# Optimization experiments

Measured on AMD Instinct MI355X. Metric: run time of the kernel, lower is better.

## Reference

```python
import jax, jax.numpy as jnp
import numpy as np

NUM_HEADS = 32
NUM_KV_HEADS = 8
HEAD_DIM = 128
HIDDEN = 4096
B, L = 2, 4096


def _phi(x):
    # feature map: elu(x) + 1
    return jax.nn.elu(x) + 1.0


def setup_inputs() -> dict:
    key = jax.random.key(0)
    ks = jax.random.split(key, 9)
    s = 1.0 / np.sqrt(HIDDEN)
    return {
        "hidden_states": jax.random.normal(ks[0], (B, L, HIDDEN), jnp.float32),
        "Wq": jax.random.normal(ks[1], (HIDDEN, HIDDEN), jnp.float32) * s,
        "bq": jnp.zeros((HIDDEN,), jnp.float32),
        "Wk": jax.random.normal(ks[2], (NUM_KV_HEADS * HEAD_DIM, HIDDEN), jnp.float32) * s,
        "bk": jnp.zeros((NUM_KV_HEADS * HEAD_DIM,), jnp.float32),
        "Wv": jax.random.normal(ks[3], (NUM_KV_HEADS * HEAD_DIM, HIDDEN), jnp.float32) * s,
        "bv": jnp.zeros((NUM_KV_HEADS * HEAD_DIM,), jnp.float32),
        "Wo": jax.random.normal(ks[4], (HIDDEN, HIDDEN), jnp.float32) * s,
        "bo": jnp.zeros((HIDDEN,), jnp.float32),
    }


def reference(hidden_states, Wq, bq, Wk, bk, Wv, bv, Wo, bo):
    bsz, q_len, _ = hidden_states.shape
    n_rep = NUM_HEADS // NUM_KV_HEADS

    # projections (nn.Linear: y = x @ W.T + b)
    q = hidden_states @ Wq.T + bq          # [B, L, H*D]
    k = hidden_states @ Wk.T + bk          # [B, L, Hkv*D]
    v = hidden_states @ Wv.T + bv

    q = q.reshape(bsz, q_len, NUM_HEADS, HEAD_DIM).transpose(0, 2, 1, 3)       # [B,H,L,D]
    k = k.reshape(bsz, q_len, NUM_KV_HEADS, HEAD_DIM).transpose(0, 2, 1, 3)    # [B,Hkv,L,D]
    v = v.reshape(bsz, q_len, NUM_KV_HEADS, HEAD_DIM).transpose(0, 2, 1, 3)

    # repeat_kv: [B,Hkv,L,D] -> [B,H,L,D]
    k = jnp.broadcast_to(k[:, :, None], (bsz, NUM_KV_HEADS, n_rep, q_len, HEAD_DIM)).reshape(bsz, NUM_HEADS, q_len, HEAD_DIM)
    v = jnp.broadcast_to(v[:, :, None], (bsz, NUM_KV_HEADS, n_rep, q_len, HEAD_DIM)).reshape(bsz, NUM_HEADS, q_len, HEAD_DIM)

    q = _phi(q)
    k = _phi(k)

    # global KV summary: O(L*d^2) linear attention
    key_value = jnp.einsum('bhld,bhlv->bhvd', k, v)           # [B,H,D,D]
    attn = jnp.einsum('bhqd,bhvd->bhqv', q, key_value)        # [B,H,L,D]

    # normalizer: sum of feature-mapped keys over sequence, per channel
    normalizer = k.sum(axis=2)[:, :, None, :]                  # [B,H,1,D]
    attn = attn / (normalizer + 1e-10)

    attn = attn.transpose(0, 2, 1, 3).reshape(bsz, q_len, HIDDEN)
    return attn @ Wo.T + bo
```

## Files before the change

kernel.cpp:

```cpp
#include <hip/hip_runtime.h>

#define HIDDEN 4096
#define NKV 8
#define NH 32
#define HD 128
#define BATCH 2
#define SEQ 4096
#define ROWS (BATCH*SEQ)

typedef short bf16x8 __attribute__((ext_vector_type(8)));
typedef float f32x4 __attribute__((ext_vector_type(4)));

static __device__ __forceinline__ float bf2f(unsigned short u) {
    union { unsigned int i; float f; } c; c.i = ((unsigned int)u) << 16; return c.f;
}
static __device__ __forceinline__ unsigned short f2bf(float x) {
    union { float f; unsigned int i; } c; c.f = x;
    unsigned int r = c.i + 0x7fffu + ((c.i >> 16) & 1u);
    return (unsigned short)(r >> 16);
}

static __device__ __forceinline__ void gl2lds16(const void* g, void* l) {
    __builtin_amdgcn_global_load_lds(
        (const __attribute__((address_space(1))) unsigned int*)g,
        (__attribute__((address_space(3))) unsigned int*)l, 16, 0, 0);
}

#define WGBAR() __builtin_amdgcn_s_barrier()
#define VMW(n) asm volatile("s_waitcnt vmcnt(" #n ")" ::: "memory")
#define LGKM0() asm volatile("s_waitcnt lgkmcnt(0)" ::: "memory")
#define SCHED_FENCE() __builtin_amdgcn_sched_barrier(0)

__global__ __launch_bounds__(256)
void cast_kernel(const float* __restrict__ in, unsigned short* __restrict__ out, int n4) {
    int idx = blockIdx.x * blockDim.x + threadIdx.x;
    int stride = gridDim.x * blockDim.x;
    for (int i = idx; i < n4; i += stride) {
        float4 f = ((const float4*)in)[i];
        ushort4 o;
        o.x = f2bf(f.x); o.y = f2bf(f.y); o.z = f2bf(f.z); o.w = f2bf(f.w);
        ((ushort4*)out)[i] = o;
    }
}

template<int MODE>
__global__ __launch_bounds__(512, 2)
void gemm256(const unsigned short* __restrict__ A, int lda,
             const unsigned short* __restrict__ B, int ldb,
             const float* __restrict__ bias0, const float* __restrict__ bias1,
             void* __restrict__ Cout, int M, int N, int K)
{
    __shared__ __align__(16) unsigned char sm[131072];

    const int tid = threadIdx.x;
    const int wid = tid >> 6, lane = tid & 63;
    const int wr = wid >> 2, wc = wid & 3;
    const int lr = lane & 15, kg = lane >> 4;
    const int lswz = (lane & 7) << 4;

    int nbx = N >> 8;
    int nwg = nbx * (M >> 8);
    int cpx = nwg >> 3;
    int bid = (int)blockIdx.x;
    int wg = (bid & 7) * cpx + (bid >> 3);
    int bx = wg % nbx, by = wg / nbx;
    int rowBase = by << 8, colBase = bx << 8;

    size_t sA[2][2], sB[2][2];
#pragma unroll
    for (int h = 0; h < 2; ++h)
#pragma unroll
        for (int i = 0; i < 2; ++i) {
            int o = i * 8192 + wid * 1024 + lane * 16;
            int row = o >> 7;
            int ce = ((o & 127) ^ ((row & 7) << 4)) >> 1;
            sA[h][i] = (size_t)(rowBase + h * 128 + row) * lda + ce;
            sB[h][i] = (size_t)(colBase + h * 128 + row) * ldb + ce;
        }
    const int ldsW = wid * 1024;

    auto SA = [&](int nb, int h, int i, size_t ko) {
        gl2lds16(A + sA[h][i] + ko, sm + nb + h * 16384 + i * 8192 + ldsW);
    };
    auto SB = [&](int nb, int h, int i, size_t ko) {
        gl2lds16(B + sB[h][i] + ko, sm + nb + 32768 + h * 16384 + i * 8192 + ldsW);
    };

    const int aRd = wr * 16384 + (lr << 7);
    const int bRd = 32768 + (wc >> 1) * 16384 + (((wc & 1) * 64 + lr) << 7);
    const int kcol0 = (kg * 16) ^ lswz;
    const int kcol1 = (64 + kg * 16) ^ lswz;

    auto RA = [&](int cb, int mp, int ks) -> bf16x8 {
        return *(const bf16x8*)(sm + cb + aRd + mp * 2048 + (ks ? kcol1 : kcol0));
    };
    auto RB = [&](int cb, int n, int ks) -> bf16x8 {
        return *(const bf16x8*)(sm + cb + bRd + n * 2048 + (ks ? kcol1 : kcol0));
    };

    f32x4 acc[8][4] = {};
    bf16x8 bfr[4][2];

    auto MF = [&](bf16x8 a0, bf16x8 a1, bf16x8 a2, bf16x8 a3, int m0, int m1) {
        LGKM0();
        SCHED_FENCE();
        __builtin_amdgcn_s_setprio(1);
#pragma unroll
        for (int n = 0; n < 4; ++n) {
            acc[m0][n] = __builtin_amdgcn_mfma_f32_16x16x32_bf16(a0, bfr[n][0], acc[m0][n], 0, 0, 0);
            acc[m0][n] = __builtin_amdgcn_mfma_f32_16x16x32_bf16(a1, bfr[n][1], acc[m0][n], 0, 0, 0);
            acc[m1][n] = __builtin_amdgcn_mfma_f32_16x16x32_bf16(a2, bfr[n][0], acc[m1][n], 0, 0, 0);
            acc[m1][n] = __builtin_amdgcn_mfma_f32_16x16x32_bf16(a3, bfr[n][1], acc[m1][n], 0, 0, 0);
        }
        __builtin_amdgcn_s_setprio(0);
        SCHED_FENCE();
    };

    SB(0, 0, 0, 0); SB(0, 0, 1, 0); SB(0, 1, 0, 0); SB(0, 1, 1, 0);
    SA(0, 0, 0, 0); SA(0, 1, 0, 0); SA(0, 0, 1, 0); SA(0, 1, 1, 0);
    VMW(2);
    WGBAR();

    int cur = 0;
    size_t ko = 64;
    const int NT = K >> 6;

    for (int t = 0; t < NT - 1; ++t) {
        const int cb = cur << 16, nb = (cur ^ 1) << 16;
        bf16x8 a0 = RA(cb, 0, 0), a1 = RA(cb, 0, 1), a2 = RA(cb, 1, 0), a3 = RA(cb, 1, 1);
#pragma unroll
        for (int n = 0; n < 4; ++n) { bfr[n][0] = RB(cb, n, 0); bfr[n][1] = RB(cb, n, 1); }
        SB(nb, 0, 0, ko); SB(nb, 0, 1, ko);
        WGBAR();
        MF(a0, a1, a2, a3, 0, 1);
        WGBAR();
        a0 = RA(cb, 2, 0); a1 = RA(cb, 2, 1); a2 = RA(cb, 3, 0); a3 = RA(cb, 3, 1);
        SB(nb, 1, 0, ko); SB(nb, 1, 1, ko);
        VMW(4);
        WGBAR();
        MF(a0, a1, a2, a3, 2, 3);
        WGBAR();
        a0 = RA(cb, 4, 0); a1 = RA(cb, 4, 1); a2 = RA(cb, 5, 0); a3 = RA(cb, 5, 1);
        SA(nb, 0, 0, ko); SA(nb, 1, 0, ko);
        WGBAR();
        MF(a0, a1, a2, a3, 4, 5);
        WGBAR();
        a0 = RA(cb, 6, 0); a1 = RA(cb, 6, 1); a2 = RA(cb, 7, 0); a3 = RA(cb, 7, 1);
        SA(nb, 0, 1, ko); SA(nb, 1, 1, ko);
        VMW(2);
        WGBAR();
        MF(a0, a1, a2, a3, 6, 7);
        WGBAR();
        cur ^= 1; ko += 64;
    }
    {
        const int cb = cur << 16;
        bf16x8 a0 = RA(cb, 0, 0), a1 = RA(cb, 0, 1), a2 = RA(cb, 1, 0), a3 = RA(cb, 1, 1);
#pragma unroll
        for (int n = 0; n < 4; ++n) { bfr[n][0] = RB(cb, n, 0); bfr[n][1] = RB(cb, n, 1); }
        WGBAR();
        MF(a0, a1, a2, a3, 0, 1);
        WGBAR();
        a0 = RA(cb, 2, 0); a1 = RA(cb, 2, 1); a2 = RA(cb, 3, 0); a3 = RA(cb, 3, 1);
        VMW(0);
        WGBAR();
        MF(a0, a1, a2, a3, 2, 3);
        WGBAR();
        a0 = RA(cb, 4, 0); a1 = RA(cb, 4, 1); a2 = RA(cb, 5, 0); a3 = RA(cb, 5, 1);
        WGBAR();
        MF(a0, a1, a2, a3, 4, 5);
        WGBAR();
        a0 = RA(cb, 6, 0); a1 = RA(cb, 6, 1); a2 = RA(cb, 7, 0), a3 = RA(cb, 7, 1);
        WGBAR();
        MF(a0, a1, a2, a3, 6, 7);
    }

    int r0 = rowBase + wr * 128 + kg * 4;
    int c0 = colBase + wc * 64 + lr;
#pragma unroll
    for (int n = 0; n < 4; ++n) {
        int col = c0 + n * 16;
        float bv;
        if (MODE == 2) bv = (col < 1024) ? bias0[col] : bias1[col - 1024];
        else           bv = bias0[col];
#pragma unroll
        for (int m = 0; m < 8; ++m) {
            int row = r0 + m * 16;
#pragma unroll
            for (int r = 0; r < 4; ++r) {
                float v = acc[m][n][r] + bv;
                if (MODE == 1) v = (v > 0.f) ? v + 1.f : __expf(v);
                if (MODE == 2 && col < 1024) v = (v > 0.f) ? v + 1.f : __expf(v);
                if (MODE == 0) ((float*)Cout)[(size_t)(row + r) * N + col] = v;
                else ((unsigned short*)Cout)[(size_t)(row + r) * N + col] = f2bf(v);
            }
        }
    }
}

__global__ __launch_bounds__(256)
void kv_partial(const unsigned short* __restrict__ Kb, const unsigned short* __restrict__ Vb,
                int ld, float* __restrict__ kvp, float* __restrict__ ksp)
{
    int chunk = blockIdx.x;
    int g = blockIdx.y;
    int b = g >> 3, hkv = g & 7;
    __shared__ float kl[32][128];
    __shared__ float vl[32][128];
    int tid = threadIdx.x;
    int c0 = (tid >> 4) * 8, d0 = (tid & 15) * 8;
    float acc[8][8] = {};
    float ksacc = 0.0f;
    size_t rowBase = (size_t)b * SEQ + (size_t)chunk * 128;

    for (int sch = 0; sch < 4; ++sch) {
        __syncthreads();
        for (int t = tid; t < 512; t += 256) {
            int l = t >> 4, col = (t & 15) * 8;
            size_t off = (rowBase + sch * 32 + l) * ld + hkv * HD + col;
            uint4 kr = *(const uint4*)(Kb + off);
            uint4 vr = *(const uint4*)(Vb + off);
            unsigned int ku[4] = {kr.x, kr.y, kr.z, kr.w};
            unsigned int vu[4] = {vr.x, vr.y, vr.z, vr.w};
#pragma unroll
            for (int q = 0; q < 4; ++q) {
                kl[l][col + q * 2]     = bf2f((unsigned short)(ku[q] & 0xffff));
                kl[l][col + q * 2 + 1] = bf2f((unsigned short)(ku[q] >> 16));
                vl[l][col + q * 2]     = bf2f((unsigned short)(vu[q] & 0xffff));
                vl[l][col + q * 2 + 1] = bf2f((unsigned short)(vu[q] >> 16));
            }
        }
        __syncthreads();
        for (int l = 0; l < 32; ++l) {
            float vv[8], kk[8];
#pragma unroll
            for (int x = 0; x < 8; ++x) { vv[x] = vl[l][c0 + x]; kk[x] = kl[l][d0 + x]; }
#pragma unroll
            for (int x = 0; x < 8; ++x)
#pragma unroll
                for (int y = 0; y < 8; ++y)
                    acc[x][y] += vv[x] * kk[y];
        }
        if (tid < 128) {
            for (int l = 0; l < 32; ++l) ksacc += kl[l][tid];
        }
    }
    float* out = kvp + ((size_t)g * 32 + chunk) * (HD * HD);
#pragma unroll
    for (int x = 0; x < 8; ++x)
#pragma unroll
        for (int y = 0; y < 8; ++y)
            out[(c0 + x) * HD + d0 + y] = acc[x][y];
    if (tid < 128) ksp[((size_t)g * 32 + chunk) * HD + tid] = ksacc;
}

__global__ __launch_bounds__(256)
void kv_reduce(const float* __restrict__ kvp, const float* __restrict__ ksp,
               unsigned short* __restrict__ kvb, float* __restrict__ ksum)
{
    int slice = blockIdx.x;
    int g = blockIdx.y;
    int tid = threadIdx.x;
    int e = slice * 1024 + tid * 4;
    float4 s = {0.f, 0.f, 0.f, 0.f};
    for (int ch = 0; ch < 32; ++ch) {
        float4 p = *(const float4*)(kvp + ((size_t)g * 32 + ch) * (HD * HD) + e);
        s.x += p.x; s.y += p.y; s.z += p.z; s.w += p.w;
    }
    ushort4 o;
    o.x = f2bf(s.x); o.y = f2bf(s.y); o.z = f2bf(s.z); o.w = f2bf(s.w);
    *(ushort4*)(kvb + (size_t)g * HD * HD + e) = o;
    if (slice == 0 && tid < 128) {
        float ss = 0.f;
        for (int ch = 0; ch < 32; ++ch) ss += ksp[((size_t)g * 32 + ch) * HD + tid];
        ksum[g * HD + tid] = ss;
    }
}

__global__ __launch_bounds__(256)
void attn_gemm(const unsigned short* __restrict__ Q,
               const unsigned short* __restrict__ KV,
               const float* __restrict__ KS,
               unsigned short* __restrict__ Out)
{
    const int BK = 32;
    __shared__ unsigned short As[128 * BK];
    __shared__ unsigned short Bs[128 * BK];

    int rt = blockIdx.x;
    int h  = blockIdx.y;
    int g = (rt >> 5) * NKV + (h >> 2);
    int rowBase = rt << 7;

    const unsigned short* A = Q + (size_t)h * HD;
    const unsigned short* B = KV + (size_t)g * HD * HD;
    const float* ks = KS + g * HD;

    int tid = threadIdx.x;
    int wave = tid >> 6, lane = tid & 63;
    int wr = wave >> 1, wc = wave & 1;

    f32x4 acc[4][4] = {};

    int sr = lane >> 2;
    int sc = (lane & 3) * 8;

    const unsigned short* Aw = A + (size_t)(rowBase + wave * 32 + sr) * HIDDEN + sc;
    const unsigned short* Bw = B + (size_t)(wave * 32 + sr) * HD + sc;
    unsigned short* Asw = As + wave * 32 * BK;
    unsigned short* Bsw = Bs + wave * 32 * BK;

    int arow = (wr * 64 + (lane & 15)) * BK + (lane >> 4) * 8;
    int brow = (wc * 64 + (lane & 15)) * BK + (lane >> 4) * 8;

    for (int kt = 0; kt < HD; kt += BK) {
        gl2lds16(Aw + kt, Asw);
        gl2lds16(Aw + kt + (size_t)16 * HIDDEN, Asw + 16 * BK);
        gl2lds16(Bw + kt, Bsw);
        gl2lds16(Bw + kt + (size_t)16 * HD, Bsw + 16 * BK);
        __syncthreads();
        bf16x8 af[4], bfr[4];
#pragma unroll
        for (int i = 0; i < 4; ++i) af[i] = *(const bf16x8*)&As[arow + i * 16 * BK];
#pragma unroll
        for (int j = 0; j < 4; ++j) bfr[j] = *(const bf16x8*)&Bs[brow + j * 16 * BK];
#pragma unroll
        for (int i = 0; i < 4; ++i)
#pragma unroll
            for (int j = 0; j < 4; ++j)
                acc[i][j] = __builtin_amdgcn_mfma_f32_16x16x32_bf16(af[i], bfr[j], acc[i][j], 0, 0, 0);
        __syncthreads();
    }

    int r0 = rowBase + wr * 64 + ((lane >> 4) << 2);
    int c0 = wc * 64 + (lane & 15);
#pragma unroll
    for (int j = 0; j < 4; ++j) {
        int col = c0 + j * 16;
        float inv = 1.0f / (ks[col] + 1e-10f);
#pragma unroll
        for (int i = 0; i < 4; ++i) {
            int row = r0 + i * 16;
#pragma unroll
            for (int r = 0; r < 4; ++r) {
                float v = acc[i][j][r] * inv;
                Out[(size_t)(row + r) * HIDDEN + h * HD + col] = f2bf(v);
            }
        }
    }
}

extern "C" void kernel_launch(void* const* d_in, const int* in_sizes, int n_in,
                              void* d_out, int out_size, void* d_ws, size_t ws_size,
                              hipStream_t stream)
{
    const float* hs = (const float*)d_in[0];
    const float* Wq = (const float*)d_in[1];
    const float* bq = (const float*)d_in[2];
    const float* Wk = (const float*)d_in[3];
    const float* bk = (const float*)d_in[4];
    const float* Wv = (const float*)d_in[5];
    const float* bv = (const float*)d_in[6];
    const float* Wo = (const float*)d_in[7];
    const float* bo = (const float*)d_in[8];

    char* ws = (char*)d_ws;
    size_t off = 0;
    auto alloc = [&](size_t bytes) -> char* {
        char* p = ws + off;
        off += (bytes + 255) & ~(size_t)255;
        return p;
    };

    unsigned short* hs_b  = (unsigned short*)alloc((size_t)ROWS * HIDDEN * 2);
    unsigned short* Wq_b  = (unsigned short*)alloc((size_t)HIDDEN * HIDDEN * 2);
    unsigned short* Wkv_b = (unsigned short*)alloc((size_t)2048 * HIDDEN * 2);
    unsigned short* Wo_b  = (unsigned short*)alloc((size_t)HIDDEN * HIDDEN * 2);
    unsigned short* kvout = (unsigned short*)alloc((size_t)ROWS * 2048 * 2);
    float* ksp   = (float*)alloc((size_t)16 * 32 * HD * 4);
    unsigned short* kvb = (unsigned short*)alloc((size_t)16 * HD * HD * 2);
    float* ksum  = (float*)alloc((size_t)16 * HD * 4);

    float* kvp = (float*)Wq_b;
    unsigned short* attn_b = hs_b;
    unsigned short* q_b = (unsigned short*)d_out;

    (void)in_sizes; (void)n_in; (void)out_size; (void)ws_size;

    auto cast = [&](const float* in, unsigned short* out, size_t n) {
        int n4 = (int)(n / 4);
        int blocks = (n4 + 255) / 256;
        if (blocks > 2048) blocks = 2048;
        cast_kernel<<<dim3(blocks), dim3(256), 0, stream>>>(in, out, n4);
    };

    cast(hs, hs_b, (size_t)ROWS * HIDDEN);
    cast(Wq, Wq_b, (size_t)HIDDEN * HIDDEN);
    cast(Wk, Wkv_b, (size_t)1024 * HIDDEN);
    cast(Wv, Wkv_b + (size_t)1024 * HIDDEN, (size_t)1024 * HIDDEN);
    cast(Wo, Wo_b, (size_t)HIDDEN * HIDDEN);

    gemm256<1><<<dim3(512), dim3(512), 0, stream>>>(hs_b, HIDDEN, Wq_b, HIDDEN, bq, nullptr, q_b, ROWS, HIDDEN, HIDDEN);
    gemm256<2><<<dim3(256), dim3(512), 0, stream>>>(hs_b, HIDDEN, Wkv_b, HIDDEN, bk, bv, kvout, ROWS, 2048, HIDDEN);

    kv_partial<<<dim3(32, 16), dim3(256), 0, stream>>>(kvout, kvout + 1024, 2048, kvp, ksp);
    kv_reduce<<<dim3(16, 16), dim3(256), 0, stream>>>(kvp, ksp, kvb, ksum);

    attn_gemm<<<dim3(64, 32), dim3(256), 0, stream>>>(q_b, kvb, ksum, attn_b);

    gemm256<0><<<dim3(512), dim3(512), 0, stream>>>(attn_b, HIDDEN, Wo_b, HIDDEN, bo, nullptr, d_out, ROWS, HIDDEN, HIDDEN);
}
```

Measured before the change: 797.3 us.

## Issue all next-tile global loads upfront and use one barrier per K-step

The GEMM main loop now issues every global-to-LDS load for the next K tile at the start of each iteration and drops the many per-quarter workgroup barriers for a single vmcnt(0)+barrier at the end. LDS reads are double-buffered in registers with partial lgkmcnt waits, so MFMA work on one register set overlaps fragment loads for the next. The aim is to remove barrier stalls and expose more memory-level parallelism. In exchange there is extra register pressure from the second register set, a full vmcnt(0) drain every iteration, and a dependence on the hand-counted lgkmcnt values being correct.

```diff
diff --git a/kernel.cpp b/kernel.cpp
--- a/kernel.cpp
+++ b/kernel.cpp
@@ -28,7 +28,7 @@
 
 #define WGBAR() __builtin_amdgcn_s_barrier()
 #define VMW(n) asm volatile("s_waitcnt vmcnt(" #n ")" ::: "memory")
-#define LGKM0() asm volatile("s_waitcnt lgkmcnt(0)" ::: "memory")
+#define LGKM(n) asm volatile("s_waitcnt lgkmcnt(" #n ")" ::: "memory")
 #define SCHED_FENCE() __builtin_amdgcn_sched_barrier(0)
 
 __global__ __launch_bounds__(256)
@@ -102,7 +102,6 @@
     bf16x8 bfr[4][2];
 
     auto MF = [&](bf16x8 a0, bf16x8 a1, bf16x8 a2, bf16x8 a3, int m0, int m1) {
-        LGKM0();
         SCHED_FENCE();
         __builtin_amdgcn_s_setprio(1);
 #pragma unroll
@@ -116,10 +115,13 @@
         SCHED_FENCE();
     };
 
+    SCHED_FENCE();
     SB(0, 0, 0, 0); SB(0, 0, 1, 0); SB(0, 1, 0, 0); SB(0, 1, 1, 0);
     SA(0, 0, 0, 0); SA(0, 1, 0, 0); SA(0, 0, 1, 0); SA(0, 1, 1, 0);
-    VMW(2);
+    SCHED_FENCE();
+    VMW(0);
     WGBAR();
+    SCHED_FENCE();
 
     int cur = 0;
     size_t ko = 64;
@@ -127,30 +129,31 @@
 
     for (int t = 0; t < NT - 1; ++t) {
         const int cb = cur << 16, nb = (cur ^ 1) << 16;
+        SCHED_FENCE();
+        SB(nb, 0, 0, ko); SB(nb, 0, 1, ko); SB(nb, 1, 0, ko); SB(nb, 1, 1, ko);
+        SA(nb, 0, 0, ko); SA(nb, 1, 0, ko); SA(nb, 0, 1, ko); SA(nb, 1, 1, ko);
+        SCHED_FENCE();
         bf16x8 a0 = RA(cb, 0, 0), a1 = RA(cb, 0, 1), a2 = RA(cb, 1, 0), a3 = RA(cb, 1, 1);
 #pragma unroll
         for (int n = 0; n < 4; ++n) { bfr[n][0] = RB(cb, n, 0); bfr[n][1] = RB(cb, n, 1); }
-        SB(nb, 0, 0, ko); SB(nb, 0, 1, ko);
+        SCHED_FENCE();
+        bf16x8 b0 = RA(cb, 2, 0), b1 = RA(cb, 2, 1), b2 = RA(cb, 3, 0), b3 = RA(cb, 3, 1);
+        SCHED_FENCE();
+        LGKM(4);
+        MF(a0, a1, a2, a3, 0, 1);
+        a0 = RA(cb, 4, 0); a1 = RA(cb, 4, 1); a2 = RA(cb, 5, 0); a3 = RA(cb, 5, 1);
+        SCHED_FENCE();
+        LGKM(4);
+        MF(b0, b1, b2, b3, 2, 3);
+        b0 = RA(cb, 6, 0); b1 = RA(cb, 6, 1); b2 = RA(cb, 7, 0); b3 = RA(cb, 7, 1);
+        SCHED_FENCE();
+        LGKM(4);
+        MF(a0, a1, a2, a3, 4, 5);
+        LGKM(0);
+        MF(b0, b1, b2, b3, 6, 7);
+        VMW(0);
         WGBAR();
-        MF(a0, a1, a2, a3, 0, 1);
-        WGBAR();
-        a0 = RA(cb, 2, 0); a1 = RA(cb, 2, 1); a2 = RA(cb, 3, 0); a3 = RA(cb, 3, 1);
-        SB(nb, 1, 0, ko); SB(nb, 1, 1, ko);
-        VMW(4);
-        WGBAR();
-        MF(a0, a1, a2, a3, 2, 3);
-        WGBAR();
-        a0 = RA(cb, 4, 0); a1 = RA(cb, 4, 1); a2 = RA(cb, 5, 0); a3 = RA(cb, 5, 1);
-        SA(nb, 0, 0, ko); SA(nb, 1, 0, ko);
-        WGBAR();
-        MF(a0, a1, a2, a3, 4, 5);
-        WGBAR();
-        a0 = RA(cb, 6, 0); a1 = RA(cb, 6, 1); a2 = RA(cb, 7, 0); a3 = RA(cb, 7, 1);
-        SA(nb, 0, 1, ko); SA(nb, 1, 1, ko);
-        VMW(2);
-        WGBAR();
-        MF(a0, a1, a2, a3, 6, 7);
-        WGBAR();
+        SCHED_FENCE();
         cur ^= 1; ko += 64;
     }
     {
@@ -158,21 +161,21 @@
         bf16x8 a0 = RA(cb, 0, 0), a1 = RA(cb, 0, 1), a2 = RA(cb, 1, 0), a3 = RA(cb, 1, 1);
 #pragma unroll
         for (int n = 0; n < 4; ++n) { bfr[n][0] = RB(cb, n, 0); bfr[n][1] = RB(cb, n, 1); }
-        WGBAR();
+        SCHED_FENCE();
+        bf16x8 b0 = RA(cb, 2, 0), b1 = RA(cb, 2, 1), b2 = RA(cb, 3, 0), b3 = RA(cb, 3, 1);
+        SCHED_FENCE();
+        LGKM(4);
         MF(a0, a1, a2, a3, 0, 1);
-        WGBAR();
-        a0 = RA(cb, 2, 0); a1 = RA(cb, 2, 1); a2 = RA(cb, 3, 0); a3 = RA(cb, 3, 1);
-        VMW(0);
-        WGBAR();
-        MF(a0, a1, a2, a3, 2, 3);
-        WGBAR();
         a0 = RA(cb, 4, 0); a1 = RA(cb, 4, 1); a2 = RA(cb, 5, 0); a3 = RA(cb, 5, 1);
-        WGBAR();
+        SCHED_FENCE();
+        LGKM(4);
+        MF(b0, b1, b2, b3, 2, 3);
+        b0 = RA(cb, 6, 0); b1 = RA(cb, 6, 1); b2 = RA(cb, 7, 0); b3 = RA(cb, 7, 1);
+        SCHED_FENCE();
+        LGKM(4);
         MF(a0, a1, a2, a3, 4, 5);
-        WGBAR();
-        a0 = RA(cb, 6, 0); a1 = RA(cb, 6, 1); a2 = RA(cb, 7, 0), a3 = RA(cb, 7, 1);
-        WGBAR();
-        MF(a0, a1, a2, a3, 6, 7);
+        LGKM(0);
+        MF(b0, b1, b2, b3, 6, 7);
     }
 
     int r0 = rowBase + wr * 128 + kg * 4;
```

Measured after the change: 774.3 us. -2.9%, faster.
